# Performance work log

Hardware: AMD Instinct MI355X
Metric: run time of the kernel (lower is better)

## Reference

```python
import jax, jax.numpy as jnp
import numpy as np

IOU_THR = 0.5
SIGMA = 0.2
BETA = 0.6
EPS = 1e-8
SCORE_FLOOR = 0.01
N_BOXES = 8192
IMG = 640.0


def setup_inputs() -> dict:
    key = jax.random.key(0)
    k1, k2, k3 = jax.random.split(key, 3)
    # realistic detector output: centers in [0, 640], sizes in [5, 105]
    c = jax.random.uniform(k1, (N_BOXES, 2), dtype=jnp.float32) * IMG
    wh = jax.random.uniform(k2, (N_BOXES, 2), dtype=jnp.float32) * 100.0 + 5.0
    boxes = jnp.concatenate([c - wh / 2, c + wh / 2], axis=-1)  # [N,4] x1y1x2y2
    scores = jax.random.uniform(k3, (N_BOXES,), dtype=jnp.float32)
    return {"boxes": boxes, "scores": scores}


def pairwise_iou(b):
    # b: [N,4] -> [N,N]
    x1 = jnp.maximum(b[:, None, 0], b[None, :, 0])
    y1 = jnp.maximum(b[:, None, 1], b[None, :, 1])
    x2 = jnp.minimum(b[:, None, 2], b[None, :, 2])
    y2 = jnp.minimum(b[:, None, 3], b[None, :, 3])
    inter = jnp.clip(x2 - x1, 0) * jnp.clip(y2 - y1, 0)
    area = (b[:, 2] - b[:, 0]) * (b[:, 3] - b[:, 1])
    union = area[:, None] + area[None, :] - inter
    return inter / (union + EPS)


def diou_vec(b1, B):
    # b1: [4] pseudo-box, B: [N,4] pseudo-boxes -> DIoU [N]
    # (faithful to original: calculate_diou is called on rows of the IoU matrix,
    #  which only uses the first 4 columns as if they were box coords)
    x1 = jnp.maximum(b1[0], B[:, 0]); y1 = jnp.maximum(b1[1], B[:, 1])
    x2 = jnp.minimum(b1[2], B[:, 2]); y2 = jnp.minimum(b1[3], B[:, 3])
    inter = jnp.clip(x2 - x1, 0) * jnp.clip(y2 - y1, 0)
    a1 = (b1[2] - b1[0]) * (b1[3] - b1[1])
    a2 = (B[:, 2] - B[:, 0]) * (B[:, 3] - B[:, 1])
    iou = inter / (a1 + a2 - inter + EPS)
    cx1 = (b1[0] + b1[2]) / 2; cy1 = (b1[1] + b1[3]) / 2
    cx2 = (B[:, 0] + B[:, 2]) / 2; cy2 = (B[:, 1] + B[:, 3]) / 2
    cdist = (cx1 - cx2) ** 2 + (cy1 - cy2) ** 2
    ex1 = jnp.minimum(b1[0], B[:, 0]); ey1 = jnp.minimum(b1[1], B[:, 1])
    ex2 = jnp.maximum(b1[2], B[:, 2]); ey2 = jnp.maximum(b1[3], B[:, 3])
    edist = (ex2 - ex1) ** 2 + (ey2 - ey1) ** 2
    return iou - cdist / (edist + EPS)


def reference(boxes, scores):
    n = boxes.shape[0]
    order = jnp.argsort(-scores)              # descending score order
    b = boxes[order]
    s = scores[order]
    iou = pairwise_iou(b)                     # [N,N]
    iou_triu = iou * jnp.triu(jnp.ones((n, n), iou.dtype), k=1)
    pseudo = iou[:, :4]                       # rows of IoU matrix used as "boxes" (as in original)

    def body(carry, xs):
        keep, sc = carry
        row_triu, pbox, i = xs
        row_keep = keep[i]                    # skip row if already suppressed
        suppress = (row_triu > IOU_THR) & keep
        penalty = jnp.exp(-(row_triu ** 2) / SIGMA)
        diou = diou_vec(pbox, pseudo)
        total = jnp.minimum(penalty + diou ** 2 / BETA, 1.0)
        active = row_keep & suppress
        new_sc = jnp.where(active, sc * total, sc)
        new_keep = keep & ~(active & (new_sc < SCORE_FLOOR))
        return (new_keep, new_sc), None

    init = (jnp.ones(n, dtype=bool), s)
    (keep, sc), _ = jax.lax.scan(body, init, (iou_triu, pseudo, jnp.arange(n)))

    # map back to original index order
    scores_out = jnp.zeros_like(scores).at[order].set(sc)
    keep_out = jnp.zeros(n, dtype=bool).at[order].set(keep)
    return scores_out, keep_out
```

## Files before the change

kernel.cpp:

```cpp
#include <hip/hip_runtime.h>

#define N 8192
#define IOU_THR 0.5f
#define SIGMA 0.2f
#define BETA 0.6f
#define EPSF 1e-8f
#define SCORE_FLOOR 0.01f
#define PAIR_BUF 2048
#define TCAP 16384

__device__ __forceinline__ float iou_f(float4 a, float4 b) {
    float x1 = fmaxf(a.x, b.x);
    float y1 = fmaxf(a.y, b.y);
    float x2 = fminf(a.z, b.z);
    float y2 = fminf(a.w, b.w);
    float inter = fmaxf(x2 - x1, 0.0f) * fmaxf(y2 - y1, 0.0f);
    float aa = (a.z - a.x) * (a.w - a.y);
    float ab = (b.z - b.x) * (b.w - b.y);
    return inter / (aa + ab - inter + EPSF);
}

__device__ __forceinline__ float diou_f(float4 a, float4 b) {
    float x1 = fmaxf(a.x, b.x);
    float y1 = fmaxf(a.y, b.y);
    float x2 = fminf(a.z, b.z);
    float y2 = fminf(a.w, b.w);
    float inter = fmaxf(x2 - x1, 0.0f) * fmaxf(y2 - y1, 0.0f);
    float a1 = (a.z - a.x) * (a.w - a.y);
    float a2 = (b.z - b.x) * (b.w - b.y);
    float iou = inter / (a1 + a2 - inter + EPSF);
    float cx1 = (a.x + a.z) * 0.5f, cy1 = (a.y + a.w) * 0.5f;
    float cx2 = (b.x + b.z) * 0.5f, cy2 = (b.y + b.w) * 0.5f;
    float dx = cx1 - cx2, dy = cy1 - cy2;
    float cdist = dx * dx + dy * dy;
    float ex1 = fminf(a.x, b.x), ey1 = fminf(a.y, b.y);
    float ex2 = fmaxf(a.z, b.z), ey2 = fmaxf(a.w, b.w);
    float ew = ex2 - ex1, eh = ey2 - ey1;
    float edist = ew * ew + eh * eh;
    return iou - cdist / (edist + EPSF);
}

__global__ __launch_bounds__(256) void k_rank(const float* __restrict__ scores,
                                              int* __restrict__ rank) {
    __shared__ unsigned long long kj[256];
    int tid = threadIdx.x;
    int gj = blockIdx.x * 256 + tid;
    unsigned sbj = __float_as_uint(scores[gj]);
    kj[tid] = ((unsigned long long)(~sbj) << 32) | (unsigned)gj;
    __syncthreads();
    int gi = blockIdx.y * 256 + tid;
    unsigned sbi = __float_as_uint(scores[gi]);
    unsigned long long ki = ((unsigned long long)(~sbi) << 32) | (unsigned)gi;
    int cnt = 0;
#pragma unroll 8
    for (int q = 0; q < 256; ++q) cnt += (kj[q] < ki) ? 1 : 0;
    if (cnt) atomicAdd(&rank[gi], cnt);
}

__global__ __launch_bounds__(256) void k_scatter(const float4* __restrict__ boxes,
                                                 const float* __restrict__ scores,
                                                 const int* __restrict__ rank,
                                                 int* __restrict__ order,
                                                 float* __restrict__ s_sorted,
                                                 float4* __restrict__ b_sorted) {
    int t = blockIdx.x * 256 + threadIdx.x;
    int r = rank[t];
    order[r] = t;
    s_sorted[r] = scores[t];
    b_sorted[r] = boxes[t];
}

__global__ __launch_bounds__(256) void k_pairs(const float4* __restrict__ b,
                                               int* __restrict__ counter,
                                               int2* __restrict__ adj, int cap) {
    int tj = blockIdx.x, ti = blockIdx.y;
    if (tj < ti) return;
    __shared__ float4 bj[256];
    __shared__ float4 pj[256];
    __shared__ int2 lbuf[PAIR_BUF];
    __shared__ int lcount, lbase;
    int tid = threadIdx.x;
    if (tid == 0) lcount = 0;
    float4 t0 = b[0], t1 = b[1], t2 = b[2], t3 = b[3];
    int jbase = tj * 256;
    float4 bjv = b[jbase + tid];
    bj[tid] = bjv;
    float4 pjv;
    pjv.x = iou_f(bjv, t0); pjv.y = iou_f(bjv, t1);
    pjv.z = iou_f(bjv, t2); pjv.w = iou_f(bjv, t3);
    pj[tid] = pjv;
    __syncthreads();
    int i = ti * 256 + tid;
    float4 bi = b[i];
    float4 pi;
    pi.x = iou_f(bi, t0); pi.y = iou_f(bi, t1);
    pi.z = iou_f(bi, t2); pi.w = iou_f(bi, t3);
    for (int jj = 0; jj < 256; ++jj) {
        int j = jbase + jj;
        if (j <= i) continue;
        float v = iou_f(bi, bj[jj]);
        if (v > IOU_THR) {
            float penalty = expf(-(v * v) / SIGMA);
            float d = diou_f(pi, pj[jj]);
            float total = fminf(penalty + (d * d) / BETA, 1.0f);
            int pos = atomicAdd(&lcount, 1);
            if (pos < PAIR_BUF) {
                int2 e;
                e.x = (i << 13) | j;
                e.y = __float_as_int(total);
                lbuf[pos] = e;
            }
        }
    }
    __syncthreads();
    if (tid == 0) {
        int c = lcount;
        if (c > PAIR_BUF) c = PAIR_BUF;
        lcount = c;
        lbase = c ? atomicAdd(counter, c) : 0;
    }
    __syncthreads();
    int c = lcount, base = lbase;
    for (int t = tid; t < c; t += 256) {
        int slot = base + t;
        if (slot < cap) adj[slot] = lbuf[t];
    }
}

__global__ __launch_bounds__(512) void k_nms(const int2* __restrict__ adj,
                                             const int* __restrict__ counter,
                                             const float* __restrict__ s_sorted,
                                             const int* __restrict__ order,
                                             float* __restrict__ out, int cap) {
    __shared__ unsigned short idx16[TCAP];
    __shared__ float fac[TCAP];
    __shared__ int starts[N];
    __shared__ unsigned char state[N];
    __shared__ int wsum[8];
    int tid = threadIdx.x;
    int T = counter[0];
    if (T > cap) T = cap;
    if (T > TCAP) T = TCAP;

    for (int r = tid; r < N; r += 512) { starts[r] = 0; state[r] = 0; }
    __syncthreads();

    for (int s = 0; s < 32; ++s) {
        int g = s * 512 + tid;
        if (g < T) {
            int2 e = adj[g];
            atomicAdd(&starts[e.x & 8191], 1);
        }
    }
    __syncthreads();

    int loc[16];
    int base = tid * 16;
    int sum = 0;
#pragma unroll
    for (int q = 0; q < 16; ++q) { loc[q] = starts[base + q]; sum += loc[q]; }
    int lane = tid & 63, wv = tid >> 6;
    int v = sum;
    for (int off = 1; off < 64; off <<= 1) {
        int u = __shfl_up(v, off);
        if (lane >= off) v += u;
    }
    if (lane == 63) wsum[wv] = v;
    __syncthreads();
    if (tid < 8) {
        int x = wsum[tid];
        for (int off = 1; off < 8; off <<= 1) {
            int u = __shfl_up(x, off);
            if (tid >= off) x += u;
        }
        wsum[tid] = x;
    }
    __syncthreads();
    int excl = ((wv == 0) ? 0 : wsum[wv - 1]) + (v - sum);
#pragma unroll
    for (int q = 0; q < 16; ++q) { starts[base + q] = excl; excl += loc[q]; }
    __syncthreads();

    for (int s = 0; s < 32; ++s) {
        int g = s * 512 + tid;
        if (g < T) {
            int2 e = adj[g];
            int j = e.x & 8191;
            int i = ((unsigned)e.x) >> 13;
            int pos = atomicAdd(&starts[j], 1);
            idx16[pos] = (unsigned short)i;
            fac[pos] = __int_as_float(e.y);
        }
    }

    int iter = 0;
    while (true) {
        __syncthreads();
        int undec = 0;
        for (int k = 0; k < 16; ++k) {
            int j = k * 512 + tid;
            if (state[j]) continue;
            int s0 = j ? starts[j - 1] : 0;
            int s1 = starts[j];
            float P = s_sorted[j];
            bool any = false, unk = false;
            for (int e = s0; e < s1; ++e) {
                unsigned char st = state[idx16[e]];
                if (st == 1) { P *= fac[e]; any = true; }
                else if (st == 0) { unk = true; }
            }
            if (any && P < SCORE_FLOOR) {
                state[j] = 2;
                int oi = order[j];
                out[oi] = P;
                out[N + oi] = 0.0f;
            } else if (!unk) {
                state[j] = 1;
                int oi = order[j];
                out[oi] = P;
                out[N + oi] = 1.0f;
            } else {
                ++undec;
            }
        }
        if (__syncthreads_count(undec) == 0) break;
        if (++iter > 4096) break;
    }
}

extern "C" void kernel_launch(void* const* d_in, const int* in_sizes, int n_in,
                              void* d_out, int out_size, void* d_ws, size_t ws_size,
                              hipStream_t stream) {
    const float4* boxes = (const float4*)d_in[0];
    const float* scores = (const float*)d_in[1];
    float* out = (float*)d_out;
    char* ws = (char*)d_ws;

    int* order = (int*)(ws);
    float* s_sorted = (float*)(ws + (32 << 10));
    float4* b_sorted = (float4*)(ws + (64 << 10));
    int* rank = (int*)(ws + (192 << 10));
    int* counter = (int*)(ws + (224 << 10));
    int2* adj = (int2*)(ws + (256 << 10));

    long long avail = ((long long)ws_size - (256 << 10)) / 8;
    if (avail < 0) avail = 0;
    int cap = TCAP;
    if (avail < cap) cap = (int)avail;

    hipMemsetAsync(ws + (192 << 10), 0, 64 << 10, stream);
    hipLaunchKernelGGL(k_rank, dim3(32, 32), dim3(256), 0, stream, scores, rank);
    hipLaunchKernelGGL(k_scatter, dim3(32), dim3(256), 0, stream, boxes, scores, rank,
                       order, s_sorted, b_sorted);
    hipLaunchKernelGGL(k_pairs, dim3(32, 32), dim3(256), 0, stream, b_sorted, counter, adj, cap);
    hipLaunchKernelGGL(k_nms, dim3(1), dim3(512), 0, stream, adj, counter, s_sorted, order, out, cap);
}
```

Before: 239.4 us.

## Replace full score sort with top-4 selection and score-ordered edge orientation

```diff
diff --git a/kernel.cpp b/kernel.cpp
--- a/kernel.cpp
+++ b/kernel.cpp
@@ -40,51 +40,58 @@
     return iou - cdist / (edist + EPSF);
 }
 
-__global__ __launch_bounds__(256) void k_rank(const float* __restrict__ scores,
-                                              int* __restrict__ rank) {
-    __shared__ unsigned long long kj[256];
+__global__ __launch_bounds__(256) void k_top4(const float* __restrict__ scores,
+                                              const float4* __restrict__ boxes,
+                                              float4* __restrict__ t4,
+                                              int* __restrict__ counter) {
+    __shared__ unsigned long long red[256];
     int tid = threadIdx.x;
-    int gj = blockIdx.x * 256 + tid;
-    unsigned sbj = __float_as_uint(scores[gj]);
-    kj[tid] = ((unsigned long long)(~sbj) << 32) | (unsigned)gj;
-    __syncthreads();
-    int gi = blockIdx.y * 256 + tid;
-    unsigned sbi = __float_as_uint(scores[gi]);
-    unsigned long long ki = ((unsigned long long)(~sbi) << 32) | (unsigned)gi;
-    int cnt = 0;
-#pragma unroll 8
-    for (int q = 0; q < 256; ++q) cnt += (kj[q] < ki) ? 1 : 0;
-    if (cnt) atomicAdd(&rank[gi], cnt);
-}
-
-__global__ __launch_bounds__(256) void k_scatter(const float4* __restrict__ boxes,
-                                                 const float* __restrict__ scores,
-                                                 const int* __restrict__ rank,
-                                                 int* __restrict__ order,
-                                                 float* __restrict__ s_sorted,
-                                                 float4* __restrict__ b_sorted) {
-    int t = blockIdx.x * 256 + threadIdx.x;
-    int r = rank[t];
-    order[r] = t;
-    s_sorted[r] = scores[t];
-    b_sorted[r] = boxes[t];
+    unsigned long long sel[4];
+    for (int k = 0; k < 4; ++k) {
+        unsigned long long best = ~0ull;
+        for (int q = 0; q < 32; ++q) {
+            int i = q * 256 + tid;
+            unsigned sb = __float_as_uint(scores[i]);
+            unsigned long long key = ((unsigned long long)(~sb) << 32) | (unsigned)i;
+            bool used = false;
+            for (int m = 0; m < k; ++m) used |= (key == sel[m]);
+            if (!used && key < best) best = key;
+        }
+        red[tid] = best;
+        __syncthreads();
+        for (int off = 128; off > 0; off >>= 1) {
+            if (tid < off) {
+                unsigned long long o = red[tid + off];
+                if (o < red[tid]) red[tid] = o;
+            }
+            __syncthreads();
+        }
+        sel[k] = red[0];
+        __syncthreads();
+    }
+    if (tid < 4) t4[tid] = boxes[(unsigned)(sel[tid] & 0xffffffffull)];
+    if (tid == 0) counter[0] = 0;
 }
 
 __global__ __launch_bounds__(256) void k_pairs(const float4* __restrict__ b,
+                                               const float* __restrict__ scores,
+                                               const float4* __restrict__ t4,
                                                int* __restrict__ counter,
                                                int2* __restrict__ adj, int cap) {
     int tj = blockIdx.x, ti = blockIdx.y;
     if (tj < ti) return;
     __shared__ float4 bj[256];
     __shared__ float4 pj[256];
+    __shared__ float sj[256];
     __shared__ int2 lbuf[PAIR_BUF];
     __shared__ int lcount, lbase;
     int tid = threadIdx.x;
     if (tid == 0) lcount = 0;
-    float4 t0 = b[0], t1 = b[1], t2 = b[2], t3 = b[3];
+    float4 t0 = t4[0], t1 = t4[1], t2 = t4[2], t3 = t4[3];
     int jbase = tj * 256;
     float4 bjv = b[jbase + tid];
     bj[tid] = bjv;
+    sj[tid] = scores[jbase + tid];
     float4 pjv;
     pjv.x = iou_f(bjv, t0); pjv.y = iou_f(bjv, t1);
     pjv.z = iou_f(bjv, t2); pjv.w = iou_f(bjv, t3);
@@ -92,6 +99,7 @@
     __syncthreads();
     int i = ti * 256 + tid;
     float4 bi = b[i];
+    float si = scores[i];
     float4 pi;
     pi.x = iou_f(bi, t0); pi.y = iou_f(bi, t1);
     pi.z = iou_f(bi, t2); pi.w = iou_f(bi, t3);
@@ -103,10 +111,12 @@
             float penalty = expf(-(v * v) / SIGMA);
             float d = diou_f(pi, pj[jj]);
             float total = fminf(penalty + (d * d) / BETA, 1.0f);
+            int src, tgt;
+            if (si >= sj[jj]) { src = i; tgt = j; } else { src = j; tgt = i; }
             int pos = atomicAdd(&lcount, 1);
             if (pos < PAIR_BUF) {
                 int2 e;
-                e.x = (i << 13) | j;
+                e.x = (src << 13) | tgt;
                 e.y = __float_as_int(total);
                 lbuf[pos] = e;
             }
@@ -129,8 +139,7 @@
 
 __global__ __launch_bounds__(512) void k_nms(const int2* __restrict__ adj,
                                              const int* __restrict__ counter,
-                                             const float* __restrict__ s_sorted,
-                                             const int* __restrict__ order,
+                                             const float* __restrict__ scores,
                                              float* __restrict__ out, int cap) {
     __shared__ unsigned short idx16[TCAP];
     __shared__ float fac[TCAP];
@@ -147,18 +156,15 @@
 
     for (int s = 0; s < 32; ++s) {
         int g = s * 512 + tid;
-        if (g < T) {
-            int2 e = adj[g];
-            atomicAdd(&starts[e.x & 8191], 1);
-        }
+        if (g < T) atomicAdd(&starts[adj[g].x & 8191], 1);
     }
     __syncthreads();
 
     int loc[16];
-    int base = tid * 16;
+    int base16 = tid * 16;
     int sum = 0;
 #pragma unroll
-    for (int q = 0; q < 16; ++q) { loc[q] = starts[base + q]; sum += loc[q]; }
+    for (int q = 0; q < 16; ++q) { loc[q] = starts[base16 + q]; sum += loc[q]; }
     int lane = tid & 63, wv = tid >> 6;
     int v = sum;
     for (int off = 1; off < 64; off <<= 1) {
@@ -178,53 +184,65 @@
     __syncthreads();
     int excl = ((wv == 0) ? 0 : wsum[wv - 1]) + (v - sum);
 #pragma unroll
-    for (int q = 0; q < 16; ++q) { starts[base + q] = excl; excl += loc[q]; }
+    for (int q = 0; q < 16; ++q) { starts[base16 + q] = excl; excl += loc[q]; }
     __syncthreads();
 
     for (int s = 0; s < 32; ++s) {
         int g = s * 512 + tid;
         if (g < T) {
             int2 e = adj[g];
-            int j = e.x & 8191;
-            int i = ((unsigned)e.x) >> 13;
-            int pos = atomicAdd(&starts[j], 1);
-            idx16[pos] = (unsigned short)i;
+            int pos = atomicAdd(&starts[e.x & 8191], 1);
+            idx16[pos] = (unsigned short)(((unsigned)e.x) >> 13);
             fac[pos] = __int_as_float(e.y);
         }
+    }
+    __syncthreads();
+
+    float base[16];
+    int rs0[16], rs1[16];
+    unsigned int undec = 0xffffu;
+#pragma unroll
+    for (int k = 0; k < 16; ++k) {
+        int j = k * 512 + tid;
+        base[k] = scores[j];
+        rs1[k] = starts[j];
+        rs0[k] = j ? starts[j - 1] : 0;
     }
 
     int iter = 0;
     while (true) {
-        __syncthreads();
-        int undec = 0;
-        for (int k = 0; k < 16; ++k) {
-            int j = k * 512 + tid;
-            if (state[j]) continue;
-            int s0 = j ? starts[j - 1] : 0;
-            int s1 = starts[j];
-            float P = s_sorted[j];
-            bool any = false, unk = false;
-            for (int e = s0; e < s1; ++e) {
-                unsigned char st = state[idx16[e]];
-                if (st == 1) { P *= fac[e]; any = true; }
-                else if (st == 0) { unk = true; }
+        for (int pass = 0; pass < 4; ++pass) {
+#pragma unroll
+            for (int k = 0; k < 16; ++k) {
+                if (!(undec & (1u << k))) continue;
+                int j = k * 512 + tid;
+                float P = base[k];
+                bool unk = false, dead = false;
+                int e1 = rs1[k];
+                for (int e = rs0[k]; e < e1; ++e) {
+                    unsigned char st = state[idx16[e]];
+                    if (st == 1) {
+                        P *= fac[e];
+                        if (P < SCORE_FLOOR) { dead = true; break; }
+                    } else if (st == 0) {
+                        unk = true;
+                    }
+                }
+                if (dead) {
+                    state[j] = 2;
+                    out[j] = P;
+                    out[N + j] = 0.0f;
+                    undec &= ~(1u << k);
+                } else if (!unk) {
+                    state[j] = 1;
+                    out[j] = P;
+                    out[N + j] = 1.0f;
+                    undec &= ~(1u << k);
+                }
             }
-            if (any && P < SCORE_FLOOR) {
-                state[j] = 2;
-                int oi = order[j];
-                out[oi] = P;
-                out[N + oi] = 0.0f;
-            } else if (!unk) {
-                state[j] = 1;
-                int oi = order[j];
-                out[oi] = P;
-                out[N + oi] = 1.0f;
-            } else {
-                ++undec;
-            }
-        }
-        if (__syncthreads_count(undec) == 0) break;
-        if (++iter > 4096) break;
+        }
+        if (__syncthreads_count((int)(undec != 0u)) == 0) break;
+        if (++iter > 2048) break;
     }
 }
 
@@ -236,22 +254,18 @@
     float* out = (float*)d_out;
     char* ws = (char*)d_ws;
 
-    int* order = (int*)(ws);
-    float* s_sorted = (float*)(ws + (32 << 10));
-    float4* b_sorted = (float4*)(ws + (64 << 10));
-    int* rank = (int*)(ws + (192 << 10));
-    int* counter = (int*)(ws + (224 << 10));
-    int2* adj = (int2*)(ws + (256 << 10));
-
-    long long avail = ((long long)ws_size - (256 << 10)) / 8;
+    float4* t4 = (float4*)ws;
+    int* counter = (int*)(ws + 64);
+    int2* adj = (int2*)(ws + 4096);
+
+    long long avail = ((long long)ws_size - 4096) / 8;
     if (avail < 0) avail = 0;
     int cap = TCAP;
     if (avail < cap) cap = (int)avail;
 
-    hipMemsetAsync(ws + (192 << 10), 0, 64 << 10, stream);
-    hipLaunchKernelGGL(k_rank, dim3(32, 32), dim3(256), 0, stream, scores, rank);
-    hipLaunchKernelGGL(k_scatter, dim3(32), dim3(256), 0, stream, boxes, scores, rank,
-                       order, s_sorted, b_sorted);
-    hipLaunchKernelGGL(k_pairs, dim3(32, 32), dim3(256), 0, stream, b_sorted, counter, adj, cap);
-    hipLaunchKernelGGL(k_nms, dim3(1), dim3(512), 0, stream, adj, counter, s_sorted, order, out, cap);
-}
+    hipLaunchKernelGGL(k_top4, dim3(1), dim3(256), 0, stream, scores, boxes, t4, counter);
+    hipLaunchKernelGGL(k_pairs, dim3(32, 32), dim3(256), 0, stream,
+                       boxes, scores, t4, counter, adj, cap);
+    hipLaunchKernelGGL(k_nms, dim3(1), dim3(512), 0, stream,
+                       adj, counter, scores, out, cap);
+}
```

Result: slower. 283.8 us (+18.5%).
